# Performance work log

Measured on AMD Instinct MI355X. Metric: run time of the kernel, lower is better.

## Reference

```python
import jax, jax.numpy as jnp
import numpy as np

T, H, I, E, K = 1024, 1024, 512, 32, 4   # tokens, hidden, moe_inter, n_experts, top_k
G, TG, NS = 8, 4, 2                      # n_group, topk_group, n_shared_experts
C = 2 * T * K // E                       # expert capacity (no-drop headroom)
SCALE = 2.5                              # routed_scaling_factor


def setup_inputs() -> dict:
    key = jax.random.key(0)
    ks = jax.random.split(key, 7)
    s = 0.02
    return dict(
        hidden_states=jax.random.normal(ks[0], (T, H), jnp.float32),
        gate_w=jax.random.normal(ks[1], (E, H), jnp.float32) * s,
        e_bias=jax.random.normal(ks[2], (E,), jnp.float32) * 0.1,
        w_gate_up=jax.random.normal(ks[3], (E, 2 * I, H), jnp.float32) * s,
        w_down=jax.random.normal(ks[4], (E, H, I), jnp.float32) * s,
        w_gate_up_shared=jax.random.normal(ks[5], (2 * I * NS, H), jnp.float32) * s,
        w_down_shared=jax.random.normal(ks[6], (H, I * NS), jnp.float32) * s,
    )


def reference(hidden_states, gate_w, e_bias, w_gate_up, w_down, w_gate_up_shared, w_down_shared):
    x = hidden_states                                   # (T, H)
    # --- gate + sigmoid scoring (noaux_tc) ---
    logits = x @ gate_w.T                               # (T, E)
    scores = jax.nn.sigmoid(logits.astype(jnp.float32))
    sfc = scores + e_bias                               # scores_for_choice
    # --- group-limited top-k: top-2 sum per group, keep topk_group groups ---
    group_scores = jax.lax.top_k(sfc.reshape(T, G, E // G), 2)[0].sum(-1)  # (T, G)
    grp_idx = jax.lax.top_k(group_scores, TG)[1]        # (T, TG)
    gmask = jnp.zeros((T, G), jnp.float32).at[jnp.arange(T)[:, None], grp_idx].set(1.0)
    smask = jnp.repeat(gmask, E // G, axis=1)           # (T, E)
    sfc_m = jnp.where(smask > 0, sfc, 0.0)
    topk_idx = jax.lax.top_k(sfc_m, K)[1]               # (T, K)
    tw = jnp.take_along_axis(scores, topk_idx, axis=1)  # weights from raw scores
    tw = tw / (tw.sum(-1, keepdims=True) + 1e-20)       # norm_topk_prob
    tw = tw * SCALE
    # --- capacity-based dispatch (position within expert via cumsum of one-hot) ---
    e_flat = topk_idx.reshape(-1)                       # (T*K,)
    oh = jax.nn.one_hot(e_flat, E, dtype=jnp.float32)   # (T*K, E)
    pos = jnp.sum((jnp.cumsum(oh, axis=0) - 1.0) * oh, axis=-1).astype(jnp.int32)
    keep = (pos < C).astype(jnp.float32)                # capacity sized to never drop
    pos_c = jnp.clip(pos, 0, C - 1)
    t_flat = jnp.repeat(jnp.arange(T), K)
    combine = jnp.zeros((T, E, C), jnp.float32).at[t_flat, e_flat, pos_c].add(tw.reshape(-1) * keep)
    dispatch = jnp.zeros((T, E, C), jnp.float32).at[t_flat, e_flat, pos_c].add(keep)
    # --- grouped expert MLP (gate_up -> SiluAndMul -> down) ---
    xe = jnp.einsum('tec,th->ech', dispatch, x)         # (E, C, H)
    gu = jnp.einsum('ech,eoh->eco', xe, w_gate_up)      # (E, C, 2I)
    act = jax.nn.silu(gu[..., :I]) * gu[..., I:]
    ye = jnp.einsum('eci,ehi->ech', act, w_down)        # (E, C, H)
    routed = jnp.einsum('tec,ech->th', combine, ye)     # (T, H)
    # --- shared experts MLP on residual ---
    IS = I * NS
    gus = x @ w_gate_up_shared.T                        # (T, 2*IS)
    acts = jax.nn.silu(gus[:, :IS]) * gus[:, IS:]
    shared = acts @ w_down_shared.T                     # (T, H)
    return routed + shared
```

## Files before the change

### kernel.cpp

```cpp
#include <hip/hip_runtime.h>
#include <hip/hip_bf16.h>
#include <math.h>

#define T_TOK 1024
#define H_DIM 1024
#define I_DIM 512
#define E_NUM 32
#define K_TOP 4
#define G_NUM 8
#define TG_NUM 4
#define CAP 256
#define IS_DIM 1024
#define RSCALE 2.5f

#define MAXTILES 160

#define WS_CNT_OFF    0
#define WS_NT_OFF     128
#define WS_TILE_OFF   256
#define WS_EIDX_OFF   4096
#define WS_WN_OFF     20480
#define WS_STOK_OFF   36864
#define WS_SW_OFF     69632
#define WS_ACT_OFF    102400
#define WS_ACTS_OFF   (102400 + (size_t)E_NUM*CAP*I_DIM*2)

typedef __attribute__((ext_vector_type(8))) short short8v;
typedef __attribute__((ext_vector_type(4))) float f32x4;
typedef __attribute__((ext_vector_type(4))) unsigned uint4v;

__device__ __forceinline__ short f2bf(float f) {
    unsigned u = __float_as_uint(f);
    u += 0x7FFFu + ((u >> 16) & 1u);
    return (short)(u >> 16);
}
__device__ __forceinline__ unsigned pk2bf(float a, float b) {
    unsigned ua = __float_as_uint(a) + 0x8000u;
    unsigned ub = __float_as_uint(b) + 0x8000u;
    return __builtin_amdgcn_perm(ub, ua, 0x07060302);
}
__device__ __forceinline__ uint4v pk8bf(float4 lo, float4 hi) {
    uint4v r; r.x = pk2bf(lo.x, lo.y); r.y = pk2bf(lo.z, lo.w);
    r.z = pk2bf(hi.x, hi.y); r.w = pk2bf(hi.z, hi.w); return r;
}
__device__ __forceinline__ float silu_(float g) { return g / (1.f + expf(-g)); }

#define LDSTRIDE 40

__global__ __launch_bounds__(256) void gate_kernel(
    const float* __restrict__ x, const float* __restrict__ gate_w,
    const float* __restrict__ e_bias,
    int* __restrict__ eidx, float* __restrict__ wnorm)
{
    __shared__ float xs[H_DIM];
    __shared__ float logits[E_NUM];
    const int t = blockIdx.x;
    const int tid = threadIdx.x;
    ((float4*)xs)[tid] = ((const float4*)(x + (size_t)t * H_DIM))[tid];
    __syncthreads();

    const int e = tid >> 3, sub = tid & 7;
    const float4* gw4 = (const float4*)(gate_w + (size_t)e * H_DIM + sub * 128);
    const float4* xr4 = (const float4*)(xs + sub * 128);
    float p = 0.f;
    #pragma unroll
    for (int h = 0; h < 32; ++h) {
        float4 a = xr4[h], b = gw4[h];
        p += a.x * b.x + a.y * b.y + a.z * b.z + a.w * b.w;
    }
    for (int off = 4; off; off >>= 1) p += __shfl_down(p, off, 8);
    if (sub == 0) logits[e] = p;
    __syncthreads();
    if (tid != 0) return;

    float sc[E_NUM], sfc[E_NUM];
    for (int i = 0; i < E_NUM; ++i) {
        sc[i] = 1.f / (1.f + expf(-logits[i]));
        sfc[i] = sc[i] + e_bias[i];
    }
    float gs[G_NUM];
    for (int g = 0; g < G_NUM; ++g) {
        float m1 = -1e30f, m2 = -1e30f;
        for (int j = 0; j < E_NUM / G_NUM; ++j) {
            float v = sfc[g * (E_NUM / G_NUM) + j];
            if (v > m1) { m2 = m1; m1 = v; } else if (v > m2) m2 = v;
        }
        gs[g] = m1 + m2;
    }
    bool gm[G_NUM];
    for (int g = 0; g < G_NUM; ++g) gm[g] = false;
    for (int it = 0; it < TG_NUM; ++it) {
        int best = -1; float bv = -1e30f;
        for (int g = 0; g < G_NUM; ++g) if (!gm[g] && gs[g] > bv) { bv = gs[g]; best = g; }
        gm[best] = true;
    }
    float sm[E_NUM];
    for (int i = 0; i < E_NUM; ++i) sm[i] = gm[i / (E_NUM / G_NUM)] ? sfc[i] : 0.0f;
    int idx[K_TOP]; float w[K_TOP]; float tsum = 0.f;
    for (int it = 0; it < K_TOP; ++it) {
        int best = 0; float bv = -1e30f;
        for (int i = 0; i < E_NUM; ++i) if (sm[i] > bv) { bv = sm[i]; best = i; }
        sm[best] = -1e30f;
        idx[it] = best; w[it] = sc[best]; tsum += w[it];
    }
    float inv = RSCALE / (tsum + 1e-20f);
    const int base = t * K_TOP;
    for (int it = 0; it < K_TOP; ++it) {
        eidx[base + it] = idx[it];
        wnorm[base + it] = w[it] * inv;
    }
}

__global__ __launch_bounds__(256) void assign_kernel(
    const int* __restrict__ eidx, const float* __restrict__ wnorm,
    int* __restrict__ cnt, int* __restrict__ slot_token, float* __restrict__ slot_w,
    int* __restrict__ ntiles, int* __restrict__ tiles)
{
    __shared__ int   se[T_TOK * K_TOP];
    __shared__ float swt[T_TOK * K_TOP];
    __shared__ int   scnt[E_NUM];
    const int tid = threadIdx.x;
    for (int i = tid; i < T_TOK * K_TOP; i += 256) { se[i] = eidx[i]; swt[i] = wnorm[i]; }
    __syncthreads();

    const int e = tid >> 3;
    const int seg = tid & 7;
    const int base = seg * 512;
    int c = 0;
    for (int i = 0; i < 512; ++i) c += (se[base + i] == e);
    int excl = 0, total = 0;
    for (int s = 0; s < 8; ++s) {
        int cs = __shfl(c, s, 8);
        total += cs;
        if (s < seg) excl += cs;
    }
    if (seg == 0) { cnt[e] = total; scnt[e] = total; }
    int pos = excl;
    for (int i = 0; i < 512; ++i) {
        if (se[base + i] == e) {
            if (pos < CAP) {
                slot_token[e * CAP + pos] = (base + i) >> 2;
                slot_w[e * CAP + pos] = swt[base + i];
            }
            ++pos;
        }
    }
    __syncthreads();
    if (tid == 0) {
        int nt = 0;
        for (int t0 = 0; t0 < T_TOK; t0 += 64) {
            tiles[nt * 4] = -1; tiles[nt * 4 + 1] = t0; tiles[nt * 4 + 2] = 64; ++nt;
        }
        for (int ee = 0; ee < E_NUM; ++ee) {
            int n = min(scnt[ee], CAP);
            for (int r = 0; r < n; r += 64) {
                tiles[nt * 4] = ee; tiles[nt * 4 + 1] = r; tiles[nt * 4 + 2] = n; ++nt;
            }
        }
        *ntiles = nt;
    }
}

#define WAVE_SETUP() \
    const int tid = threadIdx.x; const int lane = tid & 63; const int wid = tid >> 6; \
    const int wm = wid & 1, wn = wid >> 1; \
    const int lr16 = lane & 15, kc = lane >> 4; \
    const int sc_ = tid & 3, srow = tid >> 2;

#define DECL_ACC() f32x4 acc[2][4]; \
    _Pragma("unroll") for (int i_ = 0; i_ < 2; ++i_) \
    _Pragma("unroll") for (int j_ = 0; j_ < 4; ++j_) acc[i_][j_] = 0.f;

#define COMPUTE_2x4(Asb, Bsb) do { \
    short8v a_[2], b_[4]; \
    _Pragma("unroll") for (int mt = 0; mt < 2; ++mt) \
        a_[mt] = *(const short8v*)&(Asb)[(wm*32 + mt*16 + lr16)*LDSTRIDE + kc*8]; \
    _Pragma("unroll") for (int nt = 0; nt < 4; ++nt) \
        b_[nt] = *(const short8v*)&(Bsb)[(wn*64 + nt*16 + lr16)*LDSTRIDE + kc*8]; \
    _Pragma("unroll") for (int mt = 0; mt < 2; ++mt) \
    _Pragma("unroll") for (int nt = 0; nt < 4; ++nt) \
        acc[mt][nt] = __builtin_amdgcn_mfma_f32_16x16x32_bf16(a_[mt], b_[nt], acc[mt][nt], 0, 0, 0); \
} while (0)

__global__ __launch_bounds__(256, 4) void gu_all_kernel(
    const float* __restrict__ x, const float* __restrict__ w_gate_up,
    const float* __restrict__ w_gus,
    const int* __restrict__ ntiles, const int* __restrict__ tiles,
    const int* __restrict__ slot_token, const float* __restrict__ slot_w,
    short* __restrict__ act, short* __restrict__ acts)
{
    if ((int)blockIdx.y >= *ntiles) return;
    const int e  = tiles[blockIdx.y * 4];
    const int r0 = tiles[blockIdx.y * 4 + 1];
    const int ne = tiles[blockIdx.y * 4 + 2];
    const bool sh = (e < 0);
    if (!sh && blockIdx.x >= I_DIM / 64) return;
    const int col0 = blockIdx.x * 64;

    __shared__ __align__(16) short As[2][64 * LDSTRIDE];
    __shared__ __align__(16) short Bs[2][128 * LDSTRIDE];
    __shared__ int   toks[64];
    __shared__ float sws[64];

    WAVE_SETUP();
    if (tid < 64) {
        if (sh) { toks[tid] = r0 + tid; sws[tid] = 1.f; }
        else {
            int p = r0 + tid; bool v = p < ne;
            toks[tid] = v ? slot_token[e * CAP + p] : 0;
            sws[tid]  = v ? slot_w[e * CAP + p] : 0.f;
        }
    }
    __syncthreads();

    const int IDim = sh ? IS_DIM : I_DIM;
    const float* wbase = sh ? w_gus : (w_gate_up + (size_t)e * (2 * I_DIM) * H_DIM);
    const int c1 = srow + 64;
    const int wr0 = ((srow >> 4) & 1) * IDim + col0 + ((srow >> 5) << 4) + (srow & 15);
    const int wr1 = ((c1 >> 4) & 1) * IDim + col0 + ((c1 >> 5) << 4) + (c1 & 15);
    const float* aptr  = x + (size_t)toks[srow] * H_DIM + sc_ * 8;
    const float* bptr0 = wbase + (size_t)wr0 * H_DIM + sc_ * 8;
    const float* bptr1 = wbase + (size_t)wr1 * H_DIM + sc_ * 8;
    const int aoff  = srow * LDSTRIDE + sc_ * 8;
    const int boff1 = c1 * LDSTRIDE + sc_ * 8;

    DECL_ACC();
    float4 cA0 = *(const float4*)(aptr),  cA1 = *(const float4*)(aptr + 4);
    float4 cB0a = *(const float4*)(bptr0), cB0b = *(const float4*)(bptr0 + 4);
    float4 cB1a = *(const float4*)(bptr1), cB1b = *(const float4*)(bptr1 + 4);

    int buf = 0;
    for (int k0 = 0; k0 < H_DIM; k0 += 32) {
        float4 nA0, nA1, nB0a, nB0b, nB1a, nB1b;
        const int k1 = k0 + 32;
        if (k1 < H_DIM) {
            nA0 = *(const float4*)(aptr + k1);   nA1 = *(const float4*)(aptr + k1 + 4);
            nB0a = *(const float4*)(bptr0 + k1); nB0b = *(const float4*)(bptr0 + k1 + 4);
            nB1a = *(const float4*)(bptr1 + k1); nB1b = *(const float4*)(bptr1 + k1 + 4);
        }
        *(uint4v*)&As[buf][aoff]  = pk8bf(cA0, cA1);
        *(uint4v*)&Bs[buf][aoff]  = pk8bf(cB0a, cB0b);
        *(uint4v*)&Bs[buf][boff1] = pk8bf(cB1a, cB1b);
        __syncthreads();
        COMPUTE_2x4(As[buf], Bs[buf]);
        buf ^= 1;
        cA0 = nA0; cA1 = nA1; cB0a = nB0a; cB0b = nB0b; cB1a = nB1a; cB1b = nB1b;
    }

    short* rowbase = sh ? (acts + (size_t)r0 * IS_DIM)
                        : (act + ((size_t)e * CAP + r0) * I_DIM);
    #pragma unroll
    for (int mt = 0; mt < 2; ++mt) {
        #pragma unroll
        for (int q = 0; q < 2; ++q) {
            f32x4 g = acc[mt][2 * q], u = acc[mt][2 * q + 1];
            int colI = col0 + wn * 32 + q * 16 + lr16;
            #pragma unroll
            for (int i = 0; i < 4; ++i) {
                int rl = wm * 32 + mt * 16 + kc * 4 + i;
                if (rl < ne - r0 || sh) {
                    float s = sws[rl];
                    rowbase[(size_t)rl * IDim + colI] = f2bf(s * silu_(g[i]) * u[i]);
                }
            }
        }
    }
}

__global__ __launch_bounds__(256, 4) void down_all_kernel(
    const short* __restrict__ act, const short* __restrict__ acts,
    const float* __restrict__ w_down, const float* __restrict__ w_ds,
    const int* __restrict__ ntiles, const int* __restrict__ tiles,
    const int* __restrict__ slot_token, float* __restrict__ out)
{
    if ((int)blockIdx.y >= *ntiles) return;
    const int e  = tiles[blockIdx.y * 4];
    const int r0 = tiles[blockIdx.y * 4 + 1];
    const int ne = tiles[blockIdx.y * 4 + 2];
    const bool sh = (e < 0);
    const int h0 = blockIdx.x * 128;

    __shared__ __align__(16) short As[2][64 * LDSTRIDE];
    __shared__ __align__(16) short Bs[2][128 * LDSTRIDE];
    __shared__ int toks[64];

    WAVE_SETUP();
    if (tid < 64) {
        if (sh) toks[tid] = r0 + tid;
        else {
            int p = r0 + tid;
            toks[tid] = (p < ne) ? slot_token[e * CAP + p] : 0;
        }
    }
    __syncthreads();

    const int Kdim = sh ? IS_DIM : I_DIM;
    const short* abase = sh ? (acts + (size_t)(r0 + srow) * IS_DIM)
                            : (act + ((size_t)e * CAP + r0 + srow) * I_DIM);
    const float* wbase = sh ? w_ds : (w_down + (size_t)e * H_DIM * I_DIM);
    const float* bptr0 = wbase + (size_t)(h0 + srow) * Kdim + sc_ * 8;
    const float* bptr1 = wbase + (size_t)(h0 + srow + 64) * Kdim + sc_ * 8;
    const short* aptr  = abase + sc_ * 8;
    const int aoff  = srow * LDSTRIDE + sc_ * 8;
    const int boff1 = (srow + 64) * LDSTRIDE + sc_ * 8;

    DECL_ACC();
    short8v cA = *(const short8v*)(aptr);
    float4 cB0a = *(const float4*)(bptr0), cB0b = *(const float4*)(bptr0 + 4);
    float4 cB1a = *(const float4*)(bptr1), cB1b = *(const float4*)(bptr1 + 4);

    int buf = 0;
    for (int k0 = 0; k0 < Kdim; k0 += 32) {
        short8v nA; float4 nB0a, nB0b, nB1a, nB1b;
        const int k1 = k0 + 32;
        if (k1 < Kdim) {
            nA = *(const short8v*)(aptr + k1);
            nB0a = *(const float4*)(bptr0 + k1); nB0b = *(const float4*)(bptr0 + k1 + 4);
            nB1a = *(const float4*)(bptr1 + k1); nB1b = *(const float4*)(bptr1 + k1 + 4);
        }
        *(short8v*)&As[buf][aoff] = cA;
        *(uint4v*)&Bs[buf][aoff]  = pk8bf(cB0a, cB0b);
        *(uint4v*)&Bs[buf][boff1] = pk8bf(cB1a, cB1b);
        __syncthreads();
        COMPUTE_2x4(As[buf], Bs[buf]);
        buf ^= 1;
        cA = nA; cB0a = nB0a; cB0b = nB0b; cB1a = nB1a; cB1b = nB1b;
    }

    #pragma unroll
    for (int mt = 0; mt < 2; ++mt) {
        #pragma unroll
        for (int i = 0; i < 4; ++i) {
            int rl = wm * 32 + mt * 16 + kc * 4 + i;
            if (rl < ne - r0 || sh) {
                float* orow = out + (size_t)toks[rl] * H_DIM + h0 + wn * 64;
                #pragma unroll
                for (int nt = 0; nt < 4; ++nt)
                    atomicAdd(&orow[nt * 16 + lr16], acc[mt][nt][i]);
            }
        }
    }
}

extern "C" void kernel_launch(void* const* d_in, const int* in_sizes, int n_in,
                              void* d_out, int out_size, void* d_ws, size_t ws_size,
                              hipStream_t stream) {
    const float* x   = (const float*)d_in[0];
    const float* gw  = (const float*)d_in[1];
    const float* eb  = (const float*)d_in[2];
    const float* wgu = (const float*)d_in[3];
    const float* wd  = (const float*)d_in[4];
    const float* wgs = (const float*)d_in[5];
    const float* wds = (const float*)d_in[6];
    float* out = (float*)d_out;
    char* ws = (char*)d_ws;

    int*   cnt    = (int*)(ws + WS_CNT_OFF);
    int*   ntiles = (int*)(ws + WS_NT_OFF);
    int*   tiles  = (int*)(ws + WS_TILE_OFF);
    int*   eidx   = (int*)(ws + WS_EIDX_OFF);
    float* wnorm  = (float*)(ws + WS_WN_OFF);
    int*   stok   = (int*)(ws + WS_STOK_OFF);
    float* sw     = (float*)(ws + WS_SW_OFF);
    short* act    = (short*)(ws + WS_ACT_OFF);
    short* acts   = (short*)(ws + WS_ACTS_OFF);

    hipMemsetAsync(out, 0, (size_t)T_TOK * H_DIM * sizeof(float), stream);
    gate_kernel<<<T_TOK, 256, 0, stream>>>(x, gw, eb, eidx, wnorm);
    assign_kernel<<<1, 256, 0, stream>>>(eidx, wnorm, cnt, stok, sw, ntiles, tiles);
    gu_all_kernel<<<dim3(IS_DIM / 64, MAXTILES), 256, 0, stream>>>(
        x, wgu, wgs, ntiles, tiles, stok, sw, act, acts);
    down_all_kernel<<<dim3(H_DIM / 128, MAXTILES), 256, 0, stream>>>(
        act, acts, wd, wds, ntiles, tiles, stok, out);
}
```

Measured before the change: 428.0 us.

## Enlarge GEMM M-tiles to 128 rows and pre-convert activations to bf16

```diff
diff --git a/kernel.cpp b/kernel.cpp
--- a/kernel.cpp
+++ b/kernel.cpp
@@ -13,7 +13,7 @@
 #define IS_DIM 1024
 #define RSCALE 2.5f
 
-#define MAXTILES 160
+#define MAXTILES 72
 
 #define WS_CNT_OFF    0
 #define WS_NT_OFF     128
@@ -22,8 +22,9 @@
 #define WS_WN_OFF     20480
 #define WS_STOK_OFF   36864
 #define WS_SW_OFF     69632
-#define WS_ACT_OFF    102400
-#define WS_ACTS_OFF   (102400 + (size_t)E_NUM*CAP*I_DIM*2)
+#define WS_XB_OFF     102400
+#define WS_ACT_OFF    (102400 + (size_t)T_TOK*H_DIM*2)
+#define WS_ACTS_OFF   (WS_ACT_OFF + (size_t)E_NUM*CAP*I_DIM*2)
 
 typedef __attribute__((ext_vector_type(8))) short short8v;
 typedef __attribute__((ext_vector_type(4))) float f32x4;
@@ -46,6 +47,14 @@
 __device__ __forceinline__ float silu_(float g) { return g / (1.f + expf(-g)); }
 
 #define LDSTRIDE 40
+
+__global__ __launch_bounds__(256) void xconv_kernel(const float* __restrict__ x,
+                                                    short* __restrict__ xb) {
+    const int i = (blockIdx.x * 256 + threadIdx.x) * 8;
+    float4 a = *(const float4*)(x + i);
+    float4 b = *(const float4*)(x + i + 4);
+    *(uint4v*)(xb + i) = pk8bf(a, b);
+}
 
 __global__ __launch_bounds__(256) void gate_kernel(
     const float* __restrict__ x, const float* __restrict__ gate_w,
@@ -148,12 +157,12 @@
     __syncthreads();
     if (tid == 0) {
         int nt = 0;
-        for (int t0 = 0; t0 < T_TOK; t0 += 64) {
-            tiles[nt * 4] = -1; tiles[nt * 4 + 1] = t0; tiles[nt * 4 + 2] = 64; ++nt;
+        for (int t0 = 0; t0 < T_TOK; t0 += 128) {
+            tiles[nt * 4] = -1; tiles[nt * 4 + 1] = t0; tiles[nt * 4 + 2] = 128; ++nt;
         }
         for (int ee = 0; ee < E_NUM; ++ee) {
             int n = min(scnt[ee], CAP);
-            for (int r = 0; r < n; r += 64) {
+            for (int r = 0; r < n; r += 128) {
                 tiles[nt * 4] = ee; tiles[nt * 4 + 1] = r; tiles[nt * 4 + 2] = n; ++nt;
             }
         }
@@ -165,25 +174,25 @@
     const int tid = threadIdx.x; const int lane = tid & 63; const int wid = tid >> 6; \
     const int wm = wid & 1, wn = wid >> 1; \
     const int lr16 = lane & 15, kc = lane >> 4; \
-    const int sc_ = tid & 3, srow = tid >> 2;
-
-#define DECL_ACC() f32x4 acc[2][4]; \
-    _Pragma("unroll") for (int i_ = 0; i_ < 2; ++i_) \
+    const int srow = tid >> 1, kh = (tid & 1) * 16;
+
+#define DECL_ACC() f32x4 acc[4][4]; \
+    _Pragma("unroll") for (int i_ = 0; i_ < 4; ++i_) \
     _Pragma("unroll") for (int j_ = 0; j_ < 4; ++j_) acc[i_][j_] = 0.f;
 
-#define COMPUTE_2x4(Asb, Bsb) do { \
-    short8v a_[2], b_[4]; \
-    _Pragma("unroll") for (int mt = 0; mt < 2; ++mt) \
-        a_[mt] = *(const short8v*)&(Asb)[(wm*32 + mt*16 + lr16)*LDSTRIDE + kc*8]; \
+#define COMPUTE_4x4(Asb, Bsb) do { \
+    short8v a_[4], b_[4]; \
+    _Pragma("unroll") for (int mt = 0; mt < 4; ++mt) \
+        a_[mt] = *(const short8v*)&(Asb)[(wm*64 + mt*16 + lr16)*LDSTRIDE + kc*8]; \
     _Pragma("unroll") for (int nt = 0; nt < 4; ++nt) \
         b_[nt] = *(const short8v*)&(Bsb)[(wn*64 + nt*16 + lr16)*LDSTRIDE + kc*8]; \
-    _Pragma("unroll") for (int mt = 0; mt < 2; ++mt) \
+    _Pragma("unroll") for (int mt = 0; mt < 4; ++mt) \
     _Pragma("unroll") for (int nt = 0; nt < 4; ++nt) \
         acc[mt][nt] = __builtin_amdgcn_mfma_f32_16x16x32_bf16(a_[mt], b_[nt], acc[mt][nt], 0, 0, 0); \
 } while (0)
 
-__global__ __launch_bounds__(256, 4) void gu_all_kernel(
-    const float* __restrict__ x, const float* __restrict__ w_gate_up,
+__global__ __launch_bounds__(256, 3) void gu_all_kernel(
+    const short* __restrict__ xb, const float* __restrict__ w_gate_up,
     const float* __restrict__ w_gus,
     const int* __restrict__ ntiles, const int* __restrict__ tiles,
     const int* __restrict__ slot_token, const float* __restrict__ slot_w,
@@ -197,13 +206,13 @@
     if (!sh && blockIdx.x >= I_DIM / 64) return;
     const int col0 = blockIdx.x * 64;
 
-    __shared__ __align__(16) short As[2][64 * LDSTRIDE];
+    __shared__ __align__(16) short As[2][128 * LDSTRIDE];
     __shared__ __align__(16) short Bs[2][128 * LDSTRIDE];
-    __shared__ int   toks[64];
-    __shared__ float sws[64];
+    __shared__ int   toks[128];
+    __shared__ float sws[128];
 
     WAVE_SETUP();
-    if (tid < 64) {
+    if (tid < 128) {
         if (sh) { toks[tid] = r0 + tid; sws[tid] = 1.f; }
         else {
             int p = r0 + tid; bool v = p < ne;
@@ -215,50 +224,49 @@
 
     const int IDim = sh ? IS_DIM : I_DIM;
     const float* wbase = sh ? w_gus : (w_gate_up + (size_t)e * (2 * I_DIM) * H_DIM);
-    const int c1 = srow + 64;
-    const int wr0 = ((srow >> 4) & 1) * IDim + col0 + ((srow >> 5) << 4) + (srow & 15);
-    const int wr1 = ((c1 >> 4) & 1) * IDim + col0 + ((c1 >> 5) << 4) + (c1 & 15);
-    const float* aptr  = x + (size_t)toks[srow] * H_DIM + sc_ * 8;
-    const float* bptr0 = wbase + (size_t)wr0 * H_DIM + sc_ * 8;
-    const float* bptr1 = wbase + (size_t)wr1 * H_DIM + sc_ * 8;
-    const int aoff  = srow * LDSTRIDE + sc_ * 8;
-    const int boff1 = c1 * LDSTRIDE + sc_ * 8;
+    const int c = srow;
+    const int wr = ((c >> 4) & 1) * IDim + col0 + ((c >> 5) << 4) + (c & 15);
+    const short* aptr = xb + (size_t)toks[srow] * H_DIM + kh;
+    const float* bptr = wbase + (size_t)wr * H_DIM + kh;
+    const int off = srow * LDSTRIDE + kh;
 
     DECL_ACC();
-    float4 cA0 = *(const float4*)(aptr),  cA1 = *(const float4*)(aptr + 4);
-    float4 cB0a = *(const float4*)(bptr0), cB0b = *(const float4*)(bptr0 + 4);
-    float4 cB1a = *(const float4*)(bptr1), cB1b = *(const float4*)(bptr1 + 4);
+    short8v cA0 = *(const short8v*)(aptr), cA1 = *(const short8v*)(aptr + 8);
+    float4 cB0 = *(const float4*)(bptr),     cB1 = *(const float4*)(bptr + 4);
+    float4 cB2 = *(const float4*)(bptr + 8), cB3 = *(const float4*)(bptr + 12);
 
     int buf = 0;
     for (int k0 = 0; k0 < H_DIM; k0 += 32) {
-        float4 nA0, nA1, nB0a, nB0b, nB1a, nB1b;
+        short8v nA0, nA1; float4 nB0, nB1, nB2, nB3;
         const int k1 = k0 + 32;
         if (k1 < H_DIM) {
-            nA0 = *(const float4*)(aptr + k1);   nA1 = *(const float4*)(aptr + k1 + 4);
-            nB0a = *(const float4*)(bptr0 + k1); nB0b = *(const float4*)(bptr0 + k1 + 4);
-            nB1a = *(const float4*)(bptr1 + k1); nB1b = *(const float4*)(bptr1 + k1 + 4);
-        }
-        *(uint4v*)&As[buf][aoff]  = pk8bf(cA0, cA1);
-        *(uint4v*)&Bs[buf][aoff]  = pk8bf(cB0a, cB0b);
-        *(uint4v*)&Bs[buf][boff1] = pk8bf(cB1a, cB1b);
+            nA0 = *(const short8v*)(aptr + k1); nA1 = *(const short8v*)(aptr + k1 + 8);
+            nB0 = *(const float4*)(bptr + k1);     nB1 = *(const float4*)(bptr + k1 + 4);
+            nB2 = *(const float4*)(bptr + k1 + 8); nB3 = *(const float4*)(bptr + k1 + 12);
+        }
+        *(short8v*)&As[buf][off]     = cA0;
+        *(short8v*)&As[buf][off + 8] = cA1;
+        *(uint4v*)&Bs[buf][off]      = pk8bf(cB0, cB1);
+        *(uint4v*)&Bs[buf][off + 8]  = pk8bf(cB2, cB3);
         __syncthreads();
-        COMPUTE_2x4(As[buf], Bs[buf]);
+        COMPUTE_4x4(As[buf], Bs[buf]);
         buf ^= 1;
-        cA0 = nA0; cA1 = nA1; cB0a = nB0a; cB0b = nB0b; cB1a = nB1a; cB1b = nB1b;
+        cA0 = nA0; cA1 = nA1; cB0 = nB0; cB1 = nB1; cB2 = nB2; cB3 = nB3;
     }
 
     short* rowbase = sh ? (acts + (size_t)r0 * IS_DIM)
                         : (act + ((size_t)e * CAP + r0) * I_DIM);
+    const int nmax = sh ? 128 : (ne - r0);
     #pragma unroll
-    for (int mt = 0; mt < 2; ++mt) {
+    for (int mt = 0; mt < 4; ++mt) {
         #pragma unroll
         for (int q = 0; q < 2; ++q) {
             f32x4 g = acc[mt][2 * q], u = acc[mt][2 * q + 1];
             int colI = col0 + wn * 32 + q * 16 + lr16;
             #pragma unroll
             for (int i = 0; i < 4; ++i) {
-                int rl = wm * 32 + mt * 16 + kc * 4 + i;
-                if (rl < ne - r0 || sh) {
+                int rl = wm * 64 + mt * 16 + kc * 4 + i;
+                if (rl < nmax) {
                     float s = sws[rl];
                     rowbase[(size_t)rl * IDim + colI] = f2bf(s * silu_(g[i]) * u[i]);
                 }
@@ -267,7 +275,7 @@
     }
 }
 
-__global__ __launch_bounds__(256, 4) void down_all_kernel(
+__global__ __launch_bounds__(256, 3) void down_all_kernel(
     const short* __restrict__ act, const short* __restrict__ acts,
     const float* __restrict__ w_down, const float* __restrict__ w_ds,
     const int* __restrict__ ntiles, const int* __restrict__ tiles,
@@ -280,12 +288,12 @@
     const bool sh = (e < 0);
     const int h0 = blockIdx.x * 128;
 
-    __shared__ __align__(16) short As[2][64 * LDSTRIDE];
+    __shared__ __align__(16) short As[2][128 * LDSTRIDE];
     __shared__ __align__(16) short Bs[2][128 * LDSTRIDE];
-    __shared__ int toks[64];
+    __shared__ int toks[128];
 
     WAVE_SETUP();
-    if (tid < 64) {
+    if (tid < 128) {
         if (sh) toks[tid] = r0 + tid;
         else {
             int p = r0 + tid;
@@ -295,44 +303,43 @@
     __syncthreads();
 
     const int Kdim = sh ? IS_DIM : I_DIM;
-    const short* abase = sh ? (acts + (size_t)(r0 + srow) * IS_DIM)
-                            : (act + ((size_t)e * CAP + r0 + srow) * I_DIM);
-    const float* wbase = sh ? w_ds : (w_down + (size_t)e * H_DIM * I_DIM);
-    const float* bptr0 = wbase + (size_t)(h0 + srow) * Kdim + sc_ * 8;
-    const float* bptr1 = wbase + (size_t)(h0 + srow + 64) * Kdim + sc_ * 8;
-    const short* aptr  = abase + sc_ * 8;
-    const int aoff  = srow * LDSTRIDE + sc_ * 8;
-    const int boff1 = (srow + 64) * LDSTRIDE + sc_ * 8;
+    const short* aptr = (sh ? (acts + (size_t)(r0 + srow) * IS_DIM)
+                            : (act + ((size_t)e * CAP + r0 + srow) * I_DIM)) + kh;
+    const float* bptr = (sh ? w_ds : (w_down + (size_t)e * H_DIM * I_DIM))
+                        + (size_t)(h0 + srow) * Kdim + kh;
+    const int off = srow * LDSTRIDE + kh;
 
     DECL_ACC();
-    short8v cA = *(const short8v*)(aptr);
-    float4 cB0a = *(const float4*)(bptr0), cB0b = *(const float4*)(bptr0 + 4);
-    float4 cB1a = *(const float4*)(bptr1), cB1b = *(const float4*)(bptr1 + 4);
+    short8v cA0 = *(const short8v*)(aptr), cA1 = *(const short8v*)(aptr + 8);
+    float4 cB0 = *(const float4*)(bptr),     cB1 = *(const float4*)(bptr + 4);
+    float4 cB2 = *(const float4*)(bptr + 8), cB3 = *(const float4*)(bptr + 12);
 
     int buf = 0;
     for (int k0 = 0; k0 < Kdim; k0 += 32) {
-        short8v nA; float4 nB0a, nB0b, nB1a, nB1b;
+        short8v nA0, nA1; float4 nB0, nB1, nB2, nB3;
         const int k1 = k0 + 32;
         if (k1 < Kdim) {
-            nA = *(const short8v*)(aptr + k1);
-            nB0a = *(const float4*)(bptr0 + k1); nB0b = *(const float4*)(bptr0 + k1 + 4);
-            nB1a = *(const float4*)(bptr1 + k1); nB1b = *(const float4*)(bptr1 + k1 + 4);
-        }
-        *(short8v*)&As[buf][aoff] = cA;
-        *(uint4v*)&Bs[buf][aoff]  = pk8bf(cB0a, cB0b);
-        *(uint4v*)&Bs[buf][boff1] = pk8bf(cB1a, cB1b);
+            nA0 = *(const short8v*)(aptr + k1); nA1 = *(const short8v*)(aptr + k1 + 8);
+            nB0 = *(const float4*)(bptr + k1);     nB1 = *(const float4*)(bptr + k1 + 4);
+            nB2 = *(const float4*)(bptr + k1 + 8); nB3 = *(const float4*)(bptr + k1 + 12);
+        }
+        *(short8v*)&As[buf][off]     = cA0;
+        *(short8v*)&As[buf][off + 8] = cA1;
+        *(uint4v*)&Bs[buf][off]      = pk8bf(cB0, cB1);
+        *(uint4v*)&Bs[buf][off + 8]  = pk8bf(cB2, cB3);
         __syncthreads();
-        COMPUTE_2x4(As[buf], Bs[buf]);
+        COMPUTE_4x4(As[buf], Bs[buf]);
         buf ^= 1;
-        cA = nA; cB0a = nB0a; cB0b = nB0b; cB1a = nB1a; cB1b = nB1b;
-    }
-
+        cA0 = nA0; cA1 = nA1; cB0 = nB0; cB1 = nB1; cB2 = nB2; cB3 = nB3;
+    }
+
+    const int nmax = sh ? 128 : (ne - r0);
     #pragma unroll
-    for (int mt = 0; mt < 2; ++mt) {
+    for (int mt = 0; mt < 4; ++mt) {
         #pragma unroll
         for (int i = 0; i < 4; ++i) {
-            int rl = wm * 32 + mt * 16 + kc * 4 + i;
-            if (rl < ne - r0 || sh) {
+            int rl = wm * 64 + mt * 16 + kc * 4 + i;
+            if (rl < nmax) {
                 float* orow = out + (size_t)toks[rl] * H_DIM + h0 + wn * 64;
                 #pragma unroll
                 for (int nt = 0; nt < 4; ++nt)
@@ -362,14 +369,16 @@
     float* wnorm  = (float*)(ws + WS_WN_OFF);
     int*   stok   = (int*)(ws + WS_STOK_OFF);
     float* sw     = (float*)(ws + WS_SW_OFF);
+    short* xb     = (short*)(ws + WS_XB_OFF);
     short* act    = (short*)(ws + WS_ACT_OFF);
     short* acts   = (short*)(ws + WS_ACTS_OFF);
 
     hipMemsetAsync(out, 0, (size_t)T_TOK * H_DIM * sizeof(float), stream);
+    xconv_kernel<<<T_TOK * H_DIM / (256 * 8), 256, 0, stream>>>(x, xb);
     gate_kernel<<<T_TOK, 256, 0, stream>>>(x, gw, eb, eidx, wnorm);
     assign_kernel<<<1, 256, 0, stream>>>(eidx, wnorm, cnt, stok, sw, ntiles, tiles);
     gu_all_kernel<<<dim3(IS_DIM / 64, MAXTILES), 256, 0, stream>>>(
-        x, wgu, wgs, ntiles, tiles, stok, sw, act, acts);
+        xb, wgu, wgs, ntiles, tiles, stok, sw, act, acts);
     down_all_kernel<<<dim3(H_DIM / 128, MAXTILES), 256, 0, stream>>>(
         act, acts, wd, wds, ntiles, tiles, stok, out);
 }
```

Measured after the change: 429.6 us. Within noise of the previous version (+0.4%).
